# Performance work log

Measured on AMD Instinct MI355X. Metric: run time of the kernel, lower is better.

The kernel has to match this reference:

```python
import jax, jax.numpy as jnp
import numpy as np

N = 100000
E = 1600000
D = 128
L = 3  # num_layers
EPS = 1e-5


def setup_inputs() -> dict:
    key = jax.random.key(0)
    ks = jax.random.split(key, 10)
    feat = jax.random.normal(ks[0], (N, D), dtype=jnp.float32)
    src = jax.random.randint(ks[1], (E,), 0, N, dtype=jnp.int32)
    dst = jax.random.randint(ks[2], (E,), 0, N, dtype=jnp.int32)
    s = 1.0 / np.sqrt(D)
    W_pool = jax.random.uniform(ks[3], (L, D, D), jnp.float32, -s, s)
    b_pool = jax.random.uniform(ks[4], (L, D), jnp.float32, -s, s)
    W_self = jax.random.uniform(ks[5], (L, D, D), jnp.float32, -s, s)
    W_neigh = jax.random.uniform(ks[6], (L, D, D), jnp.float32, -s, s)
    bias = jnp.zeros((L, D), jnp.float32)
    gamma = jnp.ones((L, D), jnp.float32)
    beta = jnp.zeros((L, D), jnp.float32)
    return {"feat": feat, "W_pool": W_pool, "b_pool": b_pool, "W_self": W_self,
            "W_neigh": W_neigh, "bias": bias, "gamma": gamma, "beta": beta,
            "src": src, "dst": dst}


def _sage_pool_layer(h, Wp, bp, Ws, Wn, b, src_all, dst_all):
    # DGL SAGEConv(aggregator_type='pool'):
    # h_pool = relu(fc_pool(h)); neigh = max over in-edges of h_pool[src];
    # out = fc_self(h) + fc_neigh(neigh) + bias  (fc_self/fc_neigh bias-free)
    hp = jax.nn.relu(h @ Wp + bp)                      # [N, d]
    msgs = hp[src_all]                                  # [E+N, d] gather
    neigh = jax.ops.segment_max(msgs, dst_all, num_segments=N)  # [N, d]
    return h @ Ws + neigh @ Wn + b


def _bn_relu(x, g, b):
    # BatchNorm1d in training mode (batch stats, biased variance) + ReLU
    mean = jnp.mean(x, axis=0)
    var = jnp.mean(jnp.square(x - mean), axis=0)
    return jax.nn.relu((x - mean) * jax.lax.rsqrt(var + EPS) * g + b)


def reference(feat, W_pool, b_pool, W_self, W_neigh, bias, gamma, beta, src, dst):
    # dgl.add_self_loop
    loop = jnp.arange(N, dtype=src.dtype)
    src_all = jnp.concatenate([src, loop])
    dst_all = jnp.concatenate([dst, loop])
    h = feat
    for l in range(L):
        h = _sage_pool_layer(h, W_pool[l], b_pool[l], W_self[l], W_neigh[l],
                             bias[l], src_all, dst_all)
        h = _bn_relu(h, gamma[l], beta[l])
    return h
```

## Files before the change

### kernel.cpp

```cpp
#include <hip/hip_runtime.h>

#define DD 128
#define MAXB 256
#define BSH 9
#define PEB 4096
#define RB 64

typedef unsigned short u16;
typedef unsigned int   u32;
typedef __attribute__((ext_vector_type(8))) short bf16x8;
typedef __attribute__((ext_vector_type(4))) float f32x4;

union U8 { uint4 u; bf16x8 v; };

__device__ inline u16 f2bf(float x) {
  u32 u = __float_as_uint(x);
  u += 0x7fffu + ((u >> 16) & 1u);
  return (u16)(u >> 16);
}
__device__ inline float bf2f_lo(u32 w) { return __uint_as_float(w << 16); }
__device__ inline float bf2f_hi(u32 w) { return __uint_as_float(w & 0xffff0000u); }
__device__ inline u32 bmax(u32 a, u32 b) {
  u32 al = a & 0xffffu, bl = b & 0xffffu;
  u32 ah = a >> 16,     bh = b >> 16;
  u32 lo = al > bl ? al : bl;
  u32 hi = ah > bh ? ah : bh;
  return lo | (hi << 16);
}

__device__ inline uint4 fragF32(const float* __restrict__ p) {
  float4 a = *(const float4*)p;
  float4 b = *(const float4*)(p + 4);
  uint4 o;
  o.x = (u32)f2bf(a.x) | ((u32)f2bf(a.y) << 16);
  o.y = (u32)f2bf(a.z) | ((u32)f2bf(a.w) << 16);
  o.z = (u32)f2bf(b.x) | ((u32)f2bf(b.y) << 16);
  o.w = (u32)f2bf(b.z) | ((u32)f2bf(b.w) << 16);
  return o;
}

__device__ inline uint4 fragBN(const u16* __restrict__ p,
                               const float* __restrict__ sc,
                               const float* __restrict__ sh, int k0) {
  uint4 u = *(const uint4*)p;
  float4 c0 = *(const float4*)(sc + k0);
  float4 c1 = *(const float4*)(sc + k0 + 4);
  float4 h0 = *(const float4*)(sh + k0);
  float4 h1 = *(const float4*)(sh + k0 + 4);
  float y0 = fmaxf(fmaf(bf2f_lo(u.x), c0.x, h0.x), 0.f);
  float y1 = fmaxf(fmaf(bf2f_hi(u.x), c0.y, h0.y), 0.f);
  float y2 = fmaxf(fmaf(bf2f_lo(u.y), c0.z, h0.z), 0.f);
  float y3 = fmaxf(fmaf(bf2f_hi(u.y), c0.w, h0.w), 0.f);
  float y4 = fmaxf(fmaf(bf2f_lo(u.z), c1.x, h1.x), 0.f);
  float y5 = fmaxf(fmaf(bf2f_hi(u.z), c1.y, h1.y), 0.f);
  float y6 = fmaxf(fmaf(bf2f_lo(u.w), c1.z, h1.z), 0.f);
  float y7 = fmaxf(fmaf(bf2f_hi(u.w), c1.w, h1.w), 0.f);
  uint4 o;
  o.x = (u32)f2bf(y0) | ((u32)f2bf(y1) << 16);
  o.y = (u32)f2bf(y2) | ((u32)f2bf(y3) << 16);
  o.z = (u32)f2bf(y4) | ((u32)f2bf(y5) << 16);
  o.w = (u32)f2bf(y6) | ((u32)f2bf(y7) << 16);
  return o;
}

__global__ __launch_bounds__(256) void k_pack_w(
    const float* __restrict__ Wp, const float* __restrict__ Wsf,
    const float* __restrict__ Wn, u16* __restrict__ Wpk)
{
  int g = blockIdx.x * 256 + threadIdx.x;
  int m = g >> 11;
  if (m >= 9) return;
  int t = g & 2047;
  const float* W = (m < 3) ? Wp + (size_t)m * 16384
                 : (m < 6) ? Wsf + (size_t)(m - 3) * 16384
                           : Wn + (size_t)(m - 6) * 16384;
  int ks = t >> 9, nt = (t >> 6) & 7, l = t & 63;
  int kbase = ks * 32 + (l >> 4) * 8;
  int n = nt * 16 + (l & 15);
  u32 o[4];
#pragma unroll
  for (int p = 0; p < 4; p++) {
    u16 e0 = f2bf(W[(size_t)(kbase + 2 * p) * DD + n]);
    u16 e1 = f2bf(W[(size_t)(kbase + 2 * p + 1) * DD + n]);
    o[p] = (u32)e0 | ((u32)e1 << 16);
  }
  uint4* dst = (uint4*)(Wpk + (size_t)m * 16384 + (size_t)t * 8);
  *dst = make_uint4(o[0], o[1], o[2], o[3]);
}

template<int MODE>
__global__ __launch_bounds__(256, 2) void k_gemm_pool(
    const float* __restrict__ featf, const u16* __restrict__ xb,
    const u16* __restrict__ Wpk, const float* __restrict__ bvec,
    const float* __restrict__ sc, const float* __restrict__ sh,
    u16* __restrict__ hp, int nrows)
{
  const int tid = threadIdx.x;
  const int w = tid >> 6, l = tid & 63;
  const int lg = l >> 4, lm = l & 15;
  const int m0 = blockIdx.x * 128 + w * 32;

  f32x4 acc[2][8];
#pragma unroll
  for (int a = 0; a < 2; a++)
#pragma unroll
    for (int b = 0; b < 8; b++) acc[a][b] = (f32x4){0.f, 0.f, 0.f, 0.f};

  int n0 = m0 + lm;      if (n0 >= nrows) n0 = nrows - 1;
  int n1 = m0 + 16 + lm; if (n1 >= nrows) n1 = nrows - 1;
  const u16* wl = Wpk + l * 8;

#pragma unroll
  for (int ks = 0; ks < 4; ks++) {
    const int k0 = ks * 32 + lg * 8;
    U8 a0, a1;
    if (MODE == 0) {
      a0.u = fragF32(featf + (size_t)n0 * DD + k0);
      a1.u = fragF32(featf + (size_t)n1 * DD + k0);
    } else {
      a0.u = fragBN(xb + (size_t)n0 * DD + k0, sc, sh, k0);
      a1.u = fragBN(xb + (size_t)n1 * DD + k0, sc, sh, k0);
    }
#pragma unroll
    for (int nt = 0; nt < 8; nt++) {
      bf16x8 wf = *(const bf16x8*)(wl + (ks * 8 + nt) * 512);
      acc[0][nt] = __builtin_amdgcn_mfma_f32_16x16x32_bf16(wf, a0.v, acc[0][nt], 0, 0, 0);
      acc[1][nt] = __builtin_amdgcn_mfma_f32_16x16x32_bf16(wf, a1.v, acc[1][nt], 0, 0, 0);
    }
  }

#pragma unroll
  for (int mf = 0; mf < 2; mf++) {
    int node = m0 + mf * 16 + lm;
    if (node < nrows) {
      u16* dst = hp + (size_t)node * DD + lg * 4;
#pragma unroll
      for (int nt = 0; nt < 8; nt++) {
        float4 b4 = *(const float4*)(bvec + nt * 16 + lg * 4);
        f32x4 a = acc[mf][nt];
        float v0 = fmaxf(a[0] + b4.x, 0.f);
        float v1 = fmaxf(a[1] + b4.y, 0.f);
        float v2 = fmaxf(a[2] + b4.z, 0.f);
        float v3 = fmaxf(a[3] + b4.w, 0.f);
        uint2 o;
        o.x = (u32)f2bf(v0) | ((u32)f2bf(v1) << 16);
        o.y = (u32)f2bf(v2) | ((u32)f2bf(v3) << 16);
        *(uint2*)(dst + nt * 16) = o;
      }
    }
  }
}

template<int MODE>
__global__ __launch_bounds__(256, 2) void k_gemm_out(
    const float* __restrict__ featf, u16* xb,
    const u16* __restrict__ gb,
    const u16* __restrict__ WpkS, const u16* __restrict__ WpkN,
    const float* __restrict__ bvec,
    const float* __restrict__ sc, const float* __restrict__ sh,
    float* __restrict__ parts, int nrows)
{
  __shared__ float red[2 * 4 * 16 * 132];
  const int tid = threadIdx.x;
  const int w = tid >> 6, l = tid & 63;
  const int lg = l >> 4, lm = l & 15;
  const int m0 = blockIdx.x * 128 + w * 32;

  f32x4 acc[2][8];
#pragma unroll
  for (int a = 0; a < 2; a++)
#pragma unroll
    for (int b = 0; b < 8; b++) acc[a][b] = (f32x4){0.f, 0.f, 0.f, 0.f};

  int n0 = m0 + lm;      if (n0 >= nrows) n0 = nrows - 1;
  int n1 = m0 + 16 + lm; if (n1 >= nrows) n1 = nrows - 1;

#pragma unroll
  for (int ks = 0; ks < 4; ks++) {
    const int k0 = ks * 32 + lg * 8;
    U8 a0, a1;
    if (MODE == 0) {
      a0.u = fragF32(featf + (size_t)n0 * DD + k0);
      a1.u = fragF32(featf + (size_t)n1 * DD + k0);
    } else {
      a0.u = fragBN(xb + (size_t)n0 * DD + k0, sc, sh, k0);
      a1.u = fragBN(xb + (size_t)n1 * DD + k0, sc, sh, k0);
    }
    const u16* wl = WpkS + l * 8;
#pragma unroll
    for (int nt = 0; nt < 8; nt++) {
      bf16x8 wf = *(const bf16x8*)(wl + (ks * 8 + nt) * 512);
      acc[0][nt] = __builtin_amdgcn_mfma_f32_16x16x32_bf16(wf, a0.v, acc[0][nt], 0, 0, 0);
      acc[1][nt] = __builtin_amdgcn_mfma_f32_16x16x32_bf16(wf, a1.v, acc[1][nt], 0, 0, 0);
    }
  }
#pragma unroll
  for (int ks = 0; ks < 4; ks++) {
    const int k0 = ks * 32 + lg * 8;
    bf16x8 g0 = *(const bf16x8*)(gb + (size_t)n0 * DD + k0);
    bf16x8 g1 = *(const bf16x8*)(gb + (size_t)n1 * DD + k0);
    const u16* wl = WpkN + l * 8;
#pragma unroll
    for (int nt = 0; nt < 8; nt++) {
      bf16x8 wf = *(const bf16x8*)(wl + (ks * 8 + nt) * 512);
      acc[0][nt] = __builtin_amdgcn_mfma_f32_16x16x32_bf16(wf, g0, acc[0][nt], 0, 0, 0);
      acc[1][nt] = __builtin_amdgcn_mfma_f32_16x16x32_bf16(wf, g1, acc[1][nt], 0, 0, 0);
    }
  }

  const int rowbase = (w * 16 + lm) * 132;
  float msk0 = (m0 + lm < nrows) ? 1.f : 0.f;
  float msk1 = (m0 + 16 + lm < nrows) ? 1.f : 0.f;
#pragma unroll
  for (int nt = 0; nt < 8; nt++) {
    float4 b4 = *(const float4*)(bvec + nt * 16 + lg * 4);
    float bj[4] = {b4.x, b4.y, b4.z, b4.w};
    float4 sv, qv;
    float* svp = &sv.x; float* qvp = &qv.x;
#pragma unroll
    for (int j = 0; j < 4; j++) {
      float v0 = acc[0][nt][j] + bj[j];
      float v1 = acc[1][nt][j] + bj[j];
      acc[0][nt][j] = v0; acc[1][nt][j] = v1;
      svp[j] = msk0 * v0 + msk1 * v1;
      qvp[j] = msk0 * v0 * v0 + msk1 * v1 * v1;
    }
    *(float4*)&red[rowbase + nt * 16 + lg * 4] = sv;
    *(float4*)&red[8448 + rowbase + nt * 16 + lg * 4] = qv;
  }

#pragma unroll
  for (int mf = 0; mf < 2; mf++) {
    int node = m0 + mf * 16 + lm;
    if (node < nrows) {
      u16* dst = xb + (size_t)node * DD + lg * 4;
#pragma unroll
      for (int nt = 0; nt < 8; nt++) {
        f32x4 a = acc[mf][nt];
        uint2 o;
        o.x = (u32)f2bf(a[0]) | ((u32)f2bf(a[1]) << 16);
        o.y = (u32)f2bf(a[2]) | ((u32)f2bf(a[3]) << 16);
        *(uint2*)(dst + nt * 16) = o;
      }
    }
  }

  __syncthreads();
  const float* cbase = &red[(tid >> 7) * 8448 + (tid & 127)];
  float ssum = 0.f;
#pragma unroll
  for (int r = 0; r < 64; r++) ssum += cbase[r * 132];
  parts[(size_t)blockIdx.x * 256 + tid] = ssum;
}

__global__ __launch_bounds__(256) void k_red1(
    const float* __restrict__ parts, float* __restrict__ pp, int nblk)
{
  int t = threadIdx.x;
  float s = 0.f;
  for (int r = blockIdx.x; r < nblk; r += RB) s += parts[(size_t)r * 256 + t];
  pp[blockIdx.x * 256 + t] = s;
}

__global__ __launch_bounds__(256) void k_zero_i(int* p, int n) {
  int i = blockIdx.x * 256 + threadIdx.x;
  if (i < n) p[i] = 0;
}

__global__ __launch_bounds__(256) void k_histb(
    const int* __restrict__ dst, int* __restrict__ bcnt, int E)
{
  __shared__ int cnt[MAXB];
  const int e0 = blockIdx.x * PEB;
  const int e1 = min(e0 + PEB, E);
  for (int i = threadIdx.x; i < MAXB; i += 256) cnt[i] = 0;
  __syncthreads();
  for (int e = e0 + threadIdx.x; e < e1; e += 256)
    atomicAdd(&cnt[dst[e] >> BSH], 1);
  __syncthreads();
  for (int i = threadIdx.x; i < MAXB; i += 256)
    if (cnt[i]) atomicAdd(&bcnt[i], cnt[i]);
}

__global__ __launch_bounds__(256) void k_bscan(
    const int* __restrict__ bcnt, int* __restrict__ boff,
    int* __restrict__ bcur, int nbuk, int E)
{
  __shared__ int sm[256];
  int t = threadIdx.x;
  int v = (t < nbuk) ? bcnt[t] : 0;
  sm[t] = v;
  __syncthreads();
  int acc = v;
#pragma unroll
  for (int s = 1; s < 256; s <<= 1) {
    int u = (t >= s) ? sm[t - s] : 0;
    __syncthreads();
    acc += u;
    sm[t] = acc;
    __syncthreads();
  }
  if (t < nbuk) { boff[t] = acc - v; bcur[t] = acc - v; }
  if (t == 0) boff[nbuk] = E;
}

__global__ __launch_bounds__(256) void k_part(
    const int* __restrict__ src, const int* __restrict__ dst,
    int* __restrict__ bcur, int2* __restrict__ pairs, int E)
{
  __shared__ int cnt[MAXB];
  __shared__ int base[MAXB];
  const int e0 = blockIdx.x * PEB;
  const int e1 = min(e0 + PEB, E);
  for (int i = threadIdx.x; i < MAXB; i += 256) cnt[i] = 0;
  __syncthreads();
  for (int e = e0 + threadIdx.x; e < e1; e += 256)
    atomicAdd(&cnt[dst[e] >> BSH], 1);
  __syncthreads();
  for (int i = threadIdx.x; i < MAXB; i += 256) {
    int c = cnt[i];
    base[i] = c ? atomicAdd(&bcur[i], c) : 0;
    cnt[i] = 0;
  }
  __syncthreads();
  for (int e = e0 + threadIdx.x; e < e1; e += 256) {
    int d = dst[e], s = src[e];
    int b = d >> BSH;
    int r = atomicAdd(&cnt[b], 1);
    pairs[base[b] + r] = make_int2(s, d);
  }
}

__global__ __launch_bounds__(256) void k_csr(
    const int2* __restrict__ pairs, const int* __restrict__ boff,
    int* __restrict__ off, int* __restrict__ eidx, int nrows, int nbuk)
{
  __shared__ int cnt[512];
  __shared__ int ps[256];
  const int b = blockIdx.x;
  const int lo = boff[b], hi = boff[b + 1];
  const int t = threadIdx.x;
  cnt[t] = 0; cnt[t + 256] = 0;
  __syncthreads();
  for (int i = lo + t; i < hi; i += 256)
    atomicAdd(&cnt[pairs[i].y & 511], 1);
  __syncthreads();
  int c0 = cnt[2 * t], c1 = cnt[2 * t + 1];
  ps[t] = c0 + c1;
  __syncthreads();
  int acc = ps[t];
#pragma unroll
  for (int s = 1; s < 256; s <<= 1) {
    int u = (t >= s) ? ps[t - s] : 0;
    __syncthreads();
    acc += u;
    ps[t] = acc;
    __syncthreads();
  }
  int base = lo + acc - (c0 + c1);
  int node0 = (b << BSH) + 2 * t;
  if (node0 < nrows)     off[node0]     = base;
  if (node0 + 1 < nrows) off[node0 + 1] = base + c0;
  if (b == nbuk - 1 && t == 0) off[nrows] = hi;
  cnt[2 * t]     = base;
  cnt[2 * t + 1] = base + c0;
  __syncthreads();
  for (int i = lo + t; i < hi; i += 256) {
    int2 p = pairs[i];
    int pos = atomicAdd(&cnt[p.y & 511], 1);
    eidx[pos] = p.x;
  }
}

__global__ __launch_bounds__(256) void k_aggregate(
    const u32* __restrict__ hp, const int* __restrict__ off,
    const int* __restrict__ eidx, u32* __restrict__ nb, int nrows)
{
  int d = blockIdx.x * 4 + (threadIdx.x >> 6);
  if (d >= nrows) return;
  int lane = threadIdx.x & 63;
  u32 a = hp[(size_t)d * 64 + lane];
  int b = off[d], e = off[d + 1];
  int i = b;
  for (; i + 7 < e; i += 8) {
    int s0 = eidx[i],     s1 = eidx[i + 1], s2 = eidx[i + 2], s3 = eidx[i + 3];
    int s4 = eidx[i + 4], s5 = eidx[i + 5], s6 = eidx[i + 6], s7 = eidx[i + 7];
    u32 v0 = hp[(size_t)s0 * 64 + lane];
    u32 v1 = hp[(size_t)s1 * 64 + lane];
    u32 v2 = hp[(size_t)s2 * 64 + lane];
    u32 v3 = hp[(size_t)s3 * 64 + lane];
    u32 v4 = hp[(size_t)s4 * 64 + lane];
    u32 v5 = hp[(size_t)s5 * 64 + lane];
    u32 v6 = hp[(size_t)s6 * 64 + lane];
    u32 v7 = hp[(size_t)s7 * 64 + lane];
    a = bmax(a, bmax(bmax(bmax(v0, v1), bmax(v2, v3)),
                     bmax(bmax(v4, v5), bmax(v6, v7))));
  }
  for (; i + 1 < e; i += 2) {
    u32 v0 = hp[(size_t)eidx[i] * 64 + lane];
    u32 v1 = hp[(size_t)eidx[i + 1] * 64 + lane];
    a = bmax(a, bmax(v0, v1));
  }
  if (i < e) a = bmax(a, hp[(size_t)eidx[i] * 64 + lane]);
  nb[(size_t)d * 64 + lane] = a;
}

__global__ __launch_bounds__(256) void k_bn_prep(
    const float* __restrict__ pp,
    const float* __restrict__ gamma, const float* __restrict__ beta,
    float* __restrict__ sc, float* __restrict__ sh, float invN)
{
  __shared__ float sums[256];
  int t = threadIdx.x;
  float s = 0.f;
#pragma unroll
  for (int k = 0; k < RB; k++) s += pp[k * 256 + t];
  sums[t] = s;
  __syncthreads();
  if (t < 128) {
    float mean = sums[t] * invN;
    float var  = sums[128 + t] * invN - mean * mean;
    float g = gamma[t] * rsqrtf(var + 1e-5f);
    sc[t] = g;
    sh[t] = beta[t] - mean * g;
  }
}

__global__ __launch_bounds__(256) void k_bn_final(
    const u16* __restrict__ xb, float* __restrict__ out,
    const float* __restrict__ sc, const float* __restrict__ sh, int n8)
{
  int i = blockIdx.x * 256 + threadIdx.x;
  if (i >= n8) return;
  uint4 v = ((const uint4*)xb)[i];
  int f0 = (i & 15) * 8;
  float4 c0 = *(const float4*)(sc + f0);
  float4 c1 = *(const float4*)(sc + f0 + 4);
  float4 h0 = *(const float4*)(sh + f0);
  float4 h1 = *(const float4*)(sh + f0 + 4);
  float4* o = (float4*)out + 2 * (size_t)i;
  o[0] = make_float4(fmaxf(fmaf(bf2f_lo(v.x), c0.x, h0.x), 0.f),
                     fmaxf(fmaf(bf2f_hi(v.x), c0.y, h0.y), 0.f),
                     fmaxf(fmaf(bf2f_lo(v.y), c0.z, h0.z), 0.f),
                     fmaxf(fmaf(bf2f_hi(v.y), c0.w, h0.w), 0.f));
  o[1] = make_float4(fmaxf(fmaf(bf2f_lo(v.z), c1.x, h1.x), 0.f),
                     fmaxf(fmaf(bf2f_hi(v.z), c1.y, h1.y), 0.f),
                     fmaxf(fmaf(bf2f_lo(v.w), c1.z, h1.z), 0.f),
                     fmaxf(fmaf(bf2f_hi(v.w), c1.w, h1.w), 0.f));
}

extern "C" void kernel_launch(void* const* d_in, const int* in_sizes, int n_in,
                              void* d_out, int out_size, void* d_ws, size_t ws_size,
                              hipStream_t stream)
{
  const float* feat    = (const float*)d_in[0];
  const float* W_pool  = (const float*)d_in[1];
  const float* b_pool  = (const float*)d_in[2];
  const float* W_self  = (const float*)d_in[3];
  const float* W_neigh = (const float*)d_in[4];
  const float* bias    = (const float*)d_in[5];
  const float* gamma   = (const float*)d_in[6];
  const float* beta    = (const float*)d_in[7];
  const int*   src     = (const int*)d_in[8];
  const int*   dst     = (const int*)d_in[9];

  const int Nn = in_sizes[0] / DD;
  const int E  = in_sizes[8];
  float* out = (float*)d_out;

  const int gB = (Nn + 127) / 128;

  const size_t ND = (size_t)Nn * DD;
  u16*   xb    = (u16*)d_ws;
  u16*   hp    = xb + ND;
  u16*   nbuf  = hp + ND;
  u16*   Wpk   = nbuf + ND;
  float* sc    = (float*)(Wpk + 9 * 16384);
  float* sh    = sc + 128;
  float* pp    = sh + 128;
  float* parts = pp + RB * 256;
  int*   bcnt  = (int*)(parts + (size_t)gB * 256);
  int*   off   = bcnt + MAXB;
  int*   boff  = off + Nn + 2;
  int*   bcur  = boff + MAXB + 2;
  int2*  pairs = (int2*)(bcur + MAXB);
  int*   eidx  = (int*)(pairs + E);

  const int nbuk = (Nn + 511) >> BSH;
  const int pB   = (E + PEB - 1) / PEB;
  const int aggB = (Nn + 3) / 4;
  const int n8   = Nn * (DD / 8);
  const int cB   = (n8 + 255) / 256;

  k_pack_w<<<72, 256, 0, stream>>>(W_pool, W_self, W_neigh, Wpk);
  k_zero_i<<<1, 256, 0, stream>>>(bcnt, MAXB);
  k_histb<<<pB, 256, 0, stream>>>(dst, bcnt, E);
  k_bscan<<<1, 256, 0, stream>>>(bcnt, boff, bcur, nbuk, E);
  k_part<<<pB, 256, 0, stream>>>(src, dst, bcur, pairs, E);
  k_csr<<<nbuk, 256, 0, stream>>>(pairs, boff, off, eidx, Nn, nbuk);

  for (int l = 0; l < 3; l++) {
    const float* bp = b_pool + (size_t)l * DD;
    const float* bl = bias + (size_t)l * DD;
    const u16* WP = Wpk + (size_t)l * 16384;
    const u16* WS = Wpk + (size_t)(3 + l) * 16384;
    const u16* WN = Wpk + (size_t)(6 + l) * 16384;

    if (l == 0)
      k_gemm_pool<0><<<gB, 256, 0, stream>>>(feat, nullptr, WP, bp, sc, sh, hp, Nn);
    else
      k_gemm_pool<1><<<gB, 256, 0, stream>>>(nullptr, xb, WP, bp, sc, sh, hp, Nn);

    k_aggregate<<<aggB, 256, 0, stream>>>((const u32*)hp, off, eidx, (u32*)nbuf, Nn);

    if (l == 0)
      k_gemm_out<0><<<gB, 256, 0, stream>>>(feat, xb, nbuf, WS, WN, bl, sc, sh, parts, Nn);
    else
      k_gemm_out<1><<<gB, 256, 0, stream>>>(nullptr, xb, nbuf, WS, WN, bl, sc, sh, parts, Nn);

    k_red1<<<RB, 256, 0, stream>>>(parts, pp, gB);
    k_bn_prep<<<1, 256, 0, stream>>>(pp, gamma + (size_t)l * DD,
                                     beta + (size_t)l * DD, sc, sh, 1.0f / (float)Nn);
  }
  k_bn_final<<<cB, 256, 0, stream>>>(xb, out, sc, sh, n8);
  (void)n_in; (void)out_size; (void)ws_size;
}
```

Measured before the change: 456.5 us.

## Vectorize max aggregation across edge slots and halve GEMM reduction LDS

The neighbor max aggregation now has each wave split into four edge slots of 16 lanes. Each lane loads 16-byte chunks of the source row and combines them with packed u16 max instructions. Slots are merged at the end with cross-lane shuffles, which raises memory-level parallelism per wave and cuts instruction count. The output GEMM's BatchNorm partial-sum reduction reuses one half-size LDS buffer in two passes, with an extra barrier, so that launch bounds can ask for 4 blocks per CU on both GEMMs. That higher occupancy target may force register spilling.

```diff
diff --git a/kernel.cpp b/kernel.cpp
--- a/kernel.cpp
+++ b/kernel.cpp
@@ -20,12 +20,11 @@
 }
 __device__ inline float bf2f_lo(u32 w) { return __uint_as_float(w << 16); }
 __device__ inline float bf2f_hi(u32 w) { return __uint_as_float(w & 0xffff0000u); }
-__device__ inline u32 bmax(u32 a, u32 b) {
-  u32 al = a & 0xffffu, bl = b & 0xffffu;
-  u32 ah = a >> 16,     bh = b >> 16;
-  u32 lo = al > bl ? al : bl;
-  u32 hi = ah > bh ? ah : bh;
-  return lo | (hi << 16);
+
+__device__ inline u32 pkmax(u32 a, u32 b) {
+  u32 r;
+  asm("v_pk_max_u16 %0, %1, %2" : "=v"(r) : "v"(a), "v"(b));
+  return r;
 }
 
 __device__ inline uint4 fragF32(const float* __restrict__ p) {
@@ -89,7 +88,7 @@
 }
 
 template<int MODE>
-__global__ __launch_bounds__(256, 2) void k_gemm_pool(
+__global__ __launch_bounds__(256, 4) void k_gemm_pool(
     const float* __restrict__ featf, const u16* __restrict__ xb,
     const u16* __restrict__ Wpk, const float* __restrict__ bvec,
     const float* __restrict__ sc, const float* __restrict__ sh,
@@ -152,7 +151,7 @@
 }
 
 template<int MODE>
-__global__ __launch_bounds__(256, 2) void k_gemm_out(
+__global__ __launch_bounds__(256, 4) void k_gemm_out(
     const float* __restrict__ featf, u16* xb,
     const u16* __restrict__ gb,
     const u16* __restrict__ WpkS, const u16* __restrict__ WpkN,
@@ -160,7 +159,7 @@
     const float* __restrict__ sc, const float* __restrict__ sh,
     float* __restrict__ parts, int nrows)
 {
-  __shared__ float red[2 * 4 * 16 * 132];
+  __shared__ float red[64 * 132];
   const int tid = threadIdx.x;
   const int w = tid >> 6, l = tid & 63;
   const int lg = l >> 4, lm = l & 15;
@@ -208,27 +207,16 @@
     }
   }
 
-  const int rowbase = (w * 16 + lm) * 132;
-  float msk0 = (m0 + lm < nrows) ? 1.f : 0.f;
-  float msk1 = (m0 + 16 + lm < nrows) ? 1.f : 0.f;
+  const float msk0 = (m0 + lm < nrows) ? 1.f : 0.f;
+  const float msk1 = (m0 + 16 + lm < nrows) ? 1.f : 0.f;
 #pragma unroll
   for (int nt = 0; nt < 8; nt++) {
     float4 b4 = *(const float4*)(bvec + nt * 16 + lg * 4);
-    float bj[4] = {b4.x, b4.y, b4.z, b4.w};
-    float4 sv, qv;
-    float* svp = &sv.x; float* qvp = &qv.x;
-#pragma unroll
-    for (int j = 0; j < 4; j++) {
-      float v0 = acc[0][nt][j] + bj[j];
-      float v1 = acc[1][nt][j] + bj[j];
-      acc[0][nt][j] = v0; acc[1][nt][j] = v1;
-      svp[j] = msk0 * v0 + msk1 * v1;
-      qvp[j] = msk0 * v0 * v0 + msk1 * v1 * v1;
-    }
-    *(float4*)&red[rowbase + nt * 16 + lg * 4] = sv;
-    *(float4*)&red[8448 + rowbase + nt * 16 + lg * 4] = qv;
-  }
-
+    acc[0][nt][0] += b4.x; acc[0][nt][1] += b4.y;
+    acc[0][nt][2] += b4.z; acc[0][nt][3] += b4.w;
+    acc[1][nt][0] += b4.x; acc[1][nt][1] += b4.y;
+    acc[1][nt][2] += b4.z; acc[1][nt][3] += b4.w;
+  }
 #pragma unroll
   for (int mf = 0; mf < 2; mf++) {
     int node = m0 + mf * 16 + lm;
@@ -245,12 +233,40 @@
     }
   }
 
-  __syncthreads();
-  const float* cbase = &red[(tid >> 7) * 8448 + (tid & 127)];
+  const int rowbase = (w * 16 + lm) * 132;
+#pragma unroll
+  for (int nt = 0; nt < 8; nt++) {
+    float4 sv;
+    sv.x = msk0 * acc[0][nt][0] + msk1 * acc[1][nt][0];
+    sv.y = msk0 * acc[0][nt][1] + msk1 * acc[1][nt][1];
+    sv.z = msk0 * acc[0][nt][2] + msk1 * acc[1][nt][2];
+    sv.w = msk0 * acc[0][nt][3] + msk1 * acc[1][nt][3];
+    *(float4*)&red[rowbase + nt * 16 + lg * 4] = sv;
+  }
+  __syncthreads();
   float ssum = 0.f;
-#pragma unroll
-  for (int r = 0; r < 64; r++) ssum += cbase[r * 132];
-  parts[(size_t)blockIdx.x * 256 + tid] = ssum;
+  if (tid < 128) {
+#pragma unroll
+    for (int r = 0; r < 64; r++) ssum += red[r * 132 + tid];
+  }
+  __syncthreads();
+#pragma unroll
+  for (int nt = 0; nt < 8; nt++) {
+    float4 qv;
+    qv.x = msk0 * acc[0][nt][0] * acc[0][nt][0] + msk1 * acc[1][nt][0] * acc[1][nt][0];
+    qv.y = msk0 * acc[0][nt][1] * acc[0][nt][1] + msk1 * acc[1][nt][1] * acc[1][nt][1];
+    qv.z = msk0 * acc[0][nt][2] * acc[0][nt][2] + msk1 * acc[1][nt][2] * acc[1][nt][2];
+    qv.w = msk0 * acc[0][nt][3] * acc[0][nt][3] + msk1 * acc[1][nt][3] * acc[1][nt][3];
+    *(float4*)&red[rowbase + nt * 16 + lg * 4] = qv;
+  }
+  __syncthreads();
+  if (tid < 128) {
+    float qsum = 0.f;
+#pragma unroll
+    for (int r = 0; r < 64; r++) qsum += red[r * 132 + tid];
+    parts[(size_t)blockIdx.x * 256 + tid] = ssum;
+    parts[(size_t)blockIdx.x * 256 + 128 + tid] = qsum;
+  }
 }
 
 __global__ __launch_bounds__(256) void k_red1(
@@ -373,36 +389,42 @@
 }
 
 __global__ __launch_bounds__(256) void k_aggregate(
-    const u32* __restrict__ hp, const int* __restrict__ off,
-    const int* __restrict__ eidx, u32* __restrict__ nb, int nrows)
+    const uint4* __restrict__ hp4, const int* __restrict__ off,
+    const int* __restrict__ eidx, uint4* __restrict__ nb4, int nrows)
 {
   int d = blockIdx.x * 4 + (threadIdx.x >> 6);
   if (d >= nrows) return;
-  int lane = threadIdx.x & 63;
-  u32 a = hp[(size_t)d * 64 + lane];
-  int b = off[d], e = off[d + 1];
-  int i = b;
-  for (; i + 7 < e; i += 8) {
-    int s0 = eidx[i],     s1 = eidx[i + 1], s2 = eidx[i + 2], s3 = eidx[i + 3];
-    int s4 = eidx[i + 4], s5 = eidx[i + 5], s6 = eidx[i + 6], s7 = eidx[i + 7];
-    u32 v0 = hp[(size_t)s0 * 64 + lane];
-    u32 v1 = hp[(size_t)s1 * 64 + lane];
-    u32 v2 = hp[(size_t)s2 * 64 + lane];
-    u32 v3 = hp[(size_t)s3 * 64 + lane];
-    u32 v4 = hp[(size_t)s4 * 64 + lane];
-    u32 v5 = hp[(size_t)s5 * 64 + lane];
-    u32 v6 = hp[(size_t)s6 * 64 + lane];
-    u32 v7 = hp[(size_t)s7 * 64 + lane];
-    a = bmax(a, bmax(bmax(bmax(v0, v1), bmax(v2, v3)),
-                     bmax(bmax(v4, v5), bmax(v6, v7))));
-  }
-  for (; i + 1 < e; i += 2) {
-    u32 v0 = hp[(size_t)eidx[i] * 64 + lane];
-    u32 v1 = hp[(size_t)eidx[i + 1] * 64 + lane];
-    a = bmax(a, bmax(v0, v1));
-  }
-  if (i < e) a = bmax(a, hp[(size_t)eidx[i] * 64 + lane]);
-  nb[(size_t)d * 64 + lane] = a;
+  const int l = threadIdx.x & 63;
+  const int part = l & 15;
+  const int slot = l >> 4;
+  uint4 a = hp4[(size_t)d * 16 + part];
+  const int e = off[d + 1];
+  int i = off[d] + slot;
+  for (; i + 4 < e; i += 8) {
+    int s0 = eidx[i];
+    int s1 = eidx[i + 4];
+    uint4 v0 = hp4[(size_t)s0 * 16 + part];
+    uint4 v1 = hp4[(size_t)s1 * 16 + part];
+    a.x = pkmax(a.x, pkmax(v0.x, v1.x));
+    a.y = pkmax(a.y, pkmax(v0.y, v1.y));
+    a.z = pkmax(a.z, pkmax(v0.z, v1.z));
+    a.w = pkmax(a.w, pkmax(v0.w, v1.w));
+  }
+  if (i < e) {
+    int s0 = eidx[i];
+    uint4 v0 = hp4[(size_t)s0 * 16 + part];
+    a.x = pkmax(a.x, v0.x); a.y = pkmax(a.y, v0.y);
+    a.z = pkmax(a.z, v0.z); a.w = pkmax(a.w, v0.w);
+  }
+  a.x = pkmax(a.x, (u32)__shfl_xor((int)a.x, 16, 64));
+  a.y = pkmax(a.y, (u32)__shfl_xor((int)a.y, 16, 64));
+  a.z = pkmax(a.z, (u32)__shfl_xor((int)a.z, 16, 64));
+  a.w = pkmax(a.w, (u32)__shfl_xor((int)a.w, 16, 64));
+  a.x = pkmax(a.x, (u32)__shfl_xor((int)a.x, 32, 64));
+  a.y = pkmax(a.y, (u32)__shfl_xor((int)a.y, 32, 64));
+  a.z = pkmax(a.z, (u32)__shfl_xor((int)a.z, 32, 64));
+  a.w = pkmax(a.w, (u32)__shfl_xor((int)a.w, 32, 64));
+  if (slot == 0) nb4[(size_t)d * 16 + part] = a;
 }
 
 __global__ __launch_bounds__(256) void k_bn_prep(
@@ -511,7 +533,7 @@
     else
       k_gemm_pool<1><<<gB, 256, 0, stream>>>(nullptr, xb, WP, bp, sc, sh, hp, Nn);
 
-    k_aggregate<<<aggB, 256, 0, stream>>>((const u32*)hp, off, eidx, (u32*)nbuf, Nn);
+    k_aggregate<<<aggB, 256, 0, stream>>>((const uint4*)hp, off, eidx, (uint4*)nbuf, Nn);
 
     if (l == 0)
       k_gemm_out<0><<<gB, 256, 0, stream>>>(feat, xb, nbuf, WS, WN, bl, sc, sh, parts, Nn);
```

Measured after the change: 452.5 us. About the same (-0.9%).
